# Optimization experiments

Hardware: AMD Instinct MI355X
Metric: run time of the kernel (lower is better)

Reference implementation:

```python
import jax, jax.numpy as jnp
import numpy as np

B, N = 8, 256
IN_F, OUT_F = 64, 64
IN_E, OUT_E = 32, 64  # out_edges must equal out_features (batched matmul constraint)


def setup_inputs() -> dict:
    key = jax.random.key(0)
    ks = jax.random.split(key, 9)
    s = 0.05
    return {
        "A": jax.random.uniform(ks[0], (B, N, N), dtype=jnp.float32),
        "emb_node": jax.random.normal(ks[1], (B, N, IN_F), dtype=jnp.float32),
        "emb_edge": jax.random.normal(ks[2], (B, N, N, IN_E), dtype=jnp.float32),
        "W_node": jax.random.normal(ks[3], (IN_F, OUT_F), dtype=jnp.float32) * s,
        "b_node": jnp.zeros((OUT_F,), dtype=jnp.float32),
        "W_nodes": jax.random.normal(ks[4], (IN_F, OUT_F), dtype=jnp.float32) * s,
        "b_nodes": jnp.zeros((OUT_F,), dtype=jnp.float32),
        "W_edge": jax.random.normal(ks[5], (IN_E, OUT_E), dtype=jnp.float32) * s,
        "b_edge": jnp.zeros((OUT_E,), dtype=jnp.float32),
    }


def reference(A, emb_node, emb_edge, W_node, b_node, W_nodes, b_nodes, W_edge, b_edge):
    # Dense projections (last-axis matmul, like keras Dense)
    node_x = emb_node @ W_node + b_node        # [B,N,F]
    node_sx = emb_node @ W_nodes + b_nodes     # [B,N,F]
    edge_x = emb_edge @ W_edge + b_edge        # [B,N,N,E] (E == F)
    # Fused edge-weighted aggregation: original materializes A[...,None]*edge_x
    # then does a per-channel batched matmul with node_x; same math as:
    #   node_out[b,n,f] = sum_m A[b,n,m] * edge_x[b,n,m,f] * node_x[b,m,f]
    agg = jnp.einsum('bnm,bnmf,bmf->bnf', A, edge_x, node_x)
    node_out = jax.nn.relu(agg) + jax.nn.relu(node_sx)
    edge_out = jax.nn.relu(edge_x)
    return node_out, edge_out
```

## Files before the change

kernel.cpp:

```cpp
#include <hip/hip_runtime.h>

#define BB    8
#define NN    256
#define INF   64
#define OUTF  64
#define INE   32
#define OUTE  64

using f4     = __attribute__((ext_vector_type(4))) float;
using f32x4  = __attribute__((ext_vector_type(4))) float;
using bf16x8 = __attribute__((ext_vector_type(8))) short;
using us4    = __attribute__((ext_vector_type(4))) unsigned short;

__device__ float g_node_x[BB * NN * OUTF];
__device__ float g_relu_sx[BB * NN * OUTF];

static __device__ __forceinline__ unsigned short f2bf(float x) {
    unsigned u = __builtin_bit_cast(unsigned, x);
    u += 0x7fffu + ((u >> 16) & 1u);
    return (unsigned short)(u >> 16);
}

__global__ __launch_bounds__(256) void node_proj(
    const float* __restrict__ emb_node,
    const float* __restrict__ W1, const float* __restrict__ b1,
    const float* __restrict__ W2, const float* __restrict__ b2)
{
    __shared__ float sW1[64][64];
    __shared__ float sW2[64][64];
    __shared__ float sE[4][64];

    const int tid = threadIdx.x;

    const f4* w1v = (const f4*)W1;
    const f4* w2v = (const f4*)W2;
    f4* s1 = (f4*)&sW1[0][0];
    f4* s2 = (f4*)&sW2[0][0];
#pragma unroll
    for (int i = 0; i < 4; ++i) {
        s1[tid + i * 256] = w1v[tid + i * 256];
        s2[tid + i * 256] = w2v[tid + i * 256];
    }
    const int row0 = blockIdx.x * 4;
    if (tid < 64) ((f4*)&sE[0][0])[tid] = ((const f4*)(emb_node + row0 * 64))[tid];
    __syncthreads();

    const int s = tid >> 6;
    const int f = tid & 63;
    float a1 = b1[f];
    float a2 = b2[f];
#pragma unroll
    for (int k = 0; k < 64; ++k) {
        const float e = sE[s][k];
        a1 = fmaf(e, sW1[k][f], a1);
        a2 = fmaf(e, sW2[k][f], a2);
    }
    const int row = row0 + s;
    g_node_x[row * 64 + f]  = a1;
    g_relu_sx[row * 64 + f] = fmaxf(a2, 0.f);
}

__global__ __launch_bounds__(512, 4) void edge_agg(
    const float* __restrict__ A,
    const float* __restrict__ emb_edge,
    const float* __restrict__ W_edge,
    const float* __restrict__ b_edge,
    float* __restrict__ node_out,
    float* __restrict__ edge_out)
{
    __shared__ unsigned short sEb[256][32];
    __shared__ unsigned short sWt[64][32];
    __shared__ float sA[256];
    __shared__ float sRed[8][64];

    const int tid = threadIdx.x;
    const int bn  = blockIdx.x;
    const int b   = bn >> 8;

    const f4* embv = (const f4*)(emb_edge + (size_t)bn * (NN * INE));
#pragma unroll
    for (int it = 0; it < 4; ++it) {
        const int i = tid + it * 512;
        const f4 v = __builtin_nontemporal_load(embv + i);
        us4 h;
        h.x = f2bf(v.x); h.y = f2bf(v.y); h.z = f2bf(v.z); h.w = f2bf(v.w);
        *(us4*)&sEb[i >> 3][(i & 7) * 4] = h;
    }
    {
        const int f  = tid >> 3;
        const int k0 = (tid & 7) * 4;
        us4 h;
        h.x = f2bf(W_edge[(k0 + 0) * 64 + f]);
        h.y = f2bf(W_edge[(k0 + 1) * 64 + f]);
        h.z = f2bf(W_edge[(k0 + 2) * 64 + f]);
        h.w = f2bf(W_edge[(k0 + 3) * 64 + f]);
        *(us4*)&sWt[f][k0] = h;
    }
    if (tid < 64) ((f4*)sA)[tid] = ((const f4*)(A + bn * NN))[tid];

    const int wave  = tid >> 6;
    const int lane  = tid & 63;
    const int lrow  = lane >> 4;
    const int lcol  = lane & 15;
    const int mbase = wave * 32;

    float bias[4];
#pragma unroll
    for (int ft = 0; ft < 4; ++ft) bias[ft] = b_edge[ft * 16 + lcol];

    __syncthreads();

    bf16x8 afrag[2];
#pragma unroll
    for (int mt = 0; mt < 2; ++mt)
        afrag[mt] = *(const bf16x8*)&sEb[mbase + mt * 16 + lcol][lrow * 8];
    bf16x8 bfrag[4];
#pragma unroll
    for (int ft = 0; ft < 4; ++ft)
        bfrag[ft] = *(const bf16x8*)&sWt[ft * 16 + lcol][lrow * 8];

    f32x4 acc[2][4];
#pragma unroll
    for (int mt = 0; mt < 2; ++mt)
#pragma unroll
        for (int ft = 0; ft < 4; ++ft) {
            f32x4 c; c[0] = bias[ft]; c[1] = bias[ft]; c[2] = bias[ft]; c[3] = bias[ft];
            acc[mt][ft] = __builtin_amdgcn_mfma_f32_16x16x32_bf16(
                afrag[mt], bfrag[ft], c, 0, 0, 0);
        }

    const float* nx = g_node_x + b * (NN * OUTF);
    float* eoutBase = edge_out + (size_t)bn * (NN * OUTE);
    float agg[4] = {0.f, 0.f, 0.f, 0.f};
#pragma unroll
    for (int mt = 0; mt < 2; ++mt) {
#pragma unroll
        for (int r = 0; r < 4; ++r) {
            const int m = mbase + mt * 16 + lrow * 4 + r;
            const float a = sA[m];
            const float* nxr = nx + m * 64 + lcol;
            float* er = eoutBase + (size_t)m * 64 + lcol;
#pragma unroll
            for (int ft = 0; ft < 4; ++ft) {
                const float v = acc[mt][ft][r];
                __builtin_nontemporal_store(fmaxf(v, 0.f), er + ft * 16);
                agg[ft] = fmaf(a * v, nxr[ft * 16], agg[ft]);
            }
        }
    }

#pragma unroll
    for (int ft = 0; ft < 4; ++ft) {
        float v = agg[ft];
        v += __shfl_xor(v, 16);
        v += __shfl_xor(v, 32);
        agg[ft] = v;
    }
    if (lane < 16) {
#pragma unroll
        for (int ft = 0; ft < 4; ++ft) sRed[wave][ft * 16 + lane] = agg[ft];
    }
    __syncthreads();

    if (tid < 64) {
        float s = 0.f;
#pragma unroll
        for (int w = 0; w < 8; ++w) s += sRed[w][tid];
        node_out[bn * 64 + tid] = fmaxf(s, 0.f) + g_relu_sx[bn * 64 + tid];
    }
}

extern "C" void kernel_launch(void* const* d_in, const int* in_sizes, int n_in,
                              void* d_out, int out_size, void* d_ws, size_t ws_size,
                              hipStream_t stream) {
    const float* A        = (const float*)d_in[0];
    const float* emb_node = (const float*)d_in[1];
    const float* emb_edge = (const float*)d_in[2];
    const float* W_node   = (const float*)d_in[3];
    const float* b_node   = (const float*)d_in[4];
    const float* W_nodes  = (const float*)d_in[5];
    const float* b_nodes  = (const float*)d_in[6];
    const float* W_edge   = (const float*)d_in[7];
    const float* b_edge   = (const float*)d_in[8];

    float* node_out = (float*)d_out;
    float* edge_out = node_out + BB * NN * OUTF;

    node_proj<<<(BB * NN) / 4, 256, 0, stream>>>(emb_node, W_node, b_node, W_nodes, b_nodes);
    edge_agg<<<BB * NN, 512, 0, stream>>>(A, emb_edge, W_edge, b_edge, node_out, edge_out);
}
```

Measured before the change: 59.55 us.

## Load MFMA fragments directly from global and swap operands for vectorized stores

Measured after the change: 71.65 us. 20.3% more time.

```diff
diff --git a/kernel.cpp b/kernel.cpp
--- a/kernel.cpp
+++ b/kernel.cpp
@@ -5,15 +5,14 @@
 #define INF   64
 #define OUTF  64
 #define INE   32
-#define OUTE  64
 
 using f4     = __attribute__((ext_vector_type(4))) float;
 using f32x4  = __attribute__((ext_vector_type(4))) float;
 using bf16x8 = __attribute__((ext_vector_type(8))) short;
-using us4    = __attribute__((ext_vector_type(4))) unsigned short;
 
-__device__ float g_node_x[BB * NN * OUTF];
-__device__ float g_relu_sx[BB * NN * OUTF];
+__device__ float          g_node_x[BB * NN * OUTF];
+__device__ float          g_relu_sx[BB * NN * OUTF];
+__device__ unsigned short g_wtb[OUTF * INE];
 
 static __device__ __forceinline__ unsigned short f2bf(float x) {
     unsigned u = __builtin_bit_cast(unsigned, x);
@@ -24,13 +23,22 @@
 __global__ __launch_bounds__(256) void node_proj(
     const float* __restrict__ emb_node,
     const float* __restrict__ W1, const float* __restrict__ b1,
-    const float* __restrict__ W2, const float* __restrict__ b2)
+    const float* __restrict__ W2, const float* __restrict__ b2,
+    const float* __restrict__ W_edge)
 {
     __shared__ float sW1[64][64];
     __shared__ float sW2[64][64];
     __shared__ float sE[4][64];
 
     const int tid = threadIdx.x;
+
+    if (blockIdx.x == 0) {
+        const int f  = tid >> 2;
+        const int k0 = (tid & 3) * 8;
+#pragma unroll
+        for (int j = 0; j < 8; ++j)
+            g_wtb[f * INE + k0 + j] = f2bf(W_edge[(k0 + j) * OUTF + f]);
+    }
 
     const f4* w1v = (const f4*)W1;
     const f4* w2v = (const f4*)W2;
@@ -60,105 +68,96 @@
     g_relu_sx[row * 64 + f] = fmaxf(a2, 0.f);
 }
 
-__global__ __launch_bounds__(512, 4) void edge_agg(
+__global__ __launch_bounds__(512) void edge_agg(
     const float* __restrict__ A,
     const float* __restrict__ emb_edge,
-    const float* __restrict__ W_edge,
     const float* __restrict__ b_edge,
     float* __restrict__ node_out,
     float* __restrict__ edge_out)
 {
-    __shared__ unsigned short sEb[256][32];
-    __shared__ unsigned short sWt[64][32];
-    __shared__ float sA[256];
     __shared__ float sRed[8][64];
 
-    const int tid = threadIdx.x;
-    const int bn  = blockIdx.x;
-    const int b   = bn >> 8;
-
-    const f4* embv = (const f4*)(emb_edge + (size_t)bn * (NN * INE));
-#pragma unroll
-    for (int it = 0; it < 4; ++it) {
-        const int i = tid + it * 512;
-        const f4 v = __builtin_nontemporal_load(embv + i);
-        us4 h;
-        h.x = f2bf(v.x); h.y = f2bf(v.y); h.z = f2bf(v.z); h.w = f2bf(v.w);
-        *(us4*)&sEb[i >> 3][(i & 7) * 4] = h;
-    }
-    {
-        const int f  = tid >> 3;
-        const int k0 = (tid & 7) * 4;
-        us4 h;
-        h.x = f2bf(W_edge[(k0 + 0) * 64 + f]);
-        h.y = f2bf(W_edge[(k0 + 1) * 64 + f]);
-        h.z = f2bf(W_edge[(k0 + 2) * 64 + f]);
-        h.w = f2bf(W_edge[(k0 + 3) * 64 + f]);
-        *(us4*)&sWt[f][k0] = h;
-    }
-    if (tid < 64) ((f4*)sA)[tid] = ((const f4*)(A + bn * NN))[tid];
-
-    const int wave  = tid >> 6;
-    const int lane  = tid & 63;
-    const int lrow  = lane >> 4;
-    const int lcol  = lane & 15;
+    const int tid  = threadIdx.x;
+    const int bn   = blockIdx.x;
+    const int b    = bn >> 8;
+    const int wave = tid >> 6;
+    const int lane = tid & 63;
+    const int c    = lane & 15;
+    const int q    = lane >> 4;
     const int mbase = wave * 32;
 
-    float bias[4];
+    bf16x8 efrag[2];
 #pragma unroll
-    for (int ft = 0; ft < 4; ++ft) bias[ft] = b_edge[ft * 16 + lcol];
+    for (int mt = 0; mt < 2; ++mt) {
+        const float* rp = emb_edge + (size_t)bn * (NN * INE)
+                        + (mbase + mt * 16 + c) * INE + q * 8;
+        const f4 lo = __builtin_nontemporal_load((const f4*)rp);
+        const f4 hi = __builtin_nontemporal_load((const f4*)rp + 1);
+        bf16x8 e;
+        e[0] = (short)f2bf(lo.x); e[1] = (short)f2bf(lo.y);
+        e[2] = (short)f2bf(lo.z); e[3] = (short)f2bf(lo.w);
+        e[4] = (short)f2bf(hi.x); e[5] = (short)f2bf(hi.y);
+        e[6] = (short)f2bf(hi.z); e[7] = (short)f2bf(hi.w);
+        efrag[mt] = e;
+    }
 
-    __syncthreads();
-
-    bf16x8 afrag[2];
-#pragma unroll
-    for (int mt = 0; mt < 2; ++mt)
-        afrag[mt] = *(const bf16x8*)&sEb[mbase + mt * 16 + lcol][lrow * 8];
-    bf16x8 bfrag[4];
+    bf16x8 wfrag[4];
 #pragma unroll
     for (int ft = 0; ft < 4; ++ft)
-        bfrag[ft] = *(const bf16x8*)&sWt[ft * 16 + lcol][lrow * 8];
+        wfrag[ft] = *(const bf16x8*)&g_wtb[(ft * 16 + c) * INE + q * 8];
 
     f32x4 acc[2][4];
 #pragma unroll
-    for (int mt = 0; mt < 2; ++mt)
+    for (int ft = 0; ft < 4; ++ft) {
+        const f4 bias = *(const f4*)&b_edge[ft * 16 + q * 4];
+#pragma unroll
+        for (int mt = 0; mt < 2; ++mt)
+            acc[mt][ft] = __builtin_amdgcn_mfma_f32_16x16x32_bf16(
+                wfrag[ft], efrag[mt], bias, 0, 0, 0);
+    }
+
+    const float* Arow = A + bn * NN;
+    const float* nx   = g_node_x + b * (NN * OUTF);
+    float* eo = edge_out + (size_t)bn * (NN * OUTF);
+
+    f4 agg[4];
+#pragma unroll
+    for (int ft = 0; ft < 4; ++ft) { agg[ft].x = 0.f; agg[ft].y = 0.f; agg[ft].z = 0.f; agg[ft].w = 0.f; }
+
+#pragma unroll
+    for (int mt = 0; mt < 2; ++mt) {
+        const int   m = mbase + mt * 16 + c;
+        const float a = Arow[m];
 #pragma unroll
         for (int ft = 0; ft < 4; ++ft) {
-            f32x4 c; c[0] = bias[ft]; c[1] = bias[ft]; c[2] = bias[ft]; c[3] = bias[ft];
-            acc[mt][ft] = __builtin_amdgcn_mfma_f32_16x16x32_bf16(
-                afrag[mt], bfrag[ft], c, 0, 0, 0);
-        }
-
-    const float* nx = g_node_x + b * (NN * OUTF);
-    float* eoutBase = edge_out + (size_t)bn * (NN * OUTE);
-    float agg[4] = {0.f, 0.f, 0.f, 0.f};
-#pragma unroll
-    for (int mt = 0; mt < 2; ++mt) {
-#pragma unroll
-        for (int r = 0; r < 4; ++r) {
-            const int m = mbase + mt * 16 + lrow * 4 + r;
-            const float a = sA[m];
-            const float* nxr = nx + m * 64 + lcol;
-            float* er = eoutBase + (size_t)m * 64 + lcol;
-#pragma unroll
-            for (int ft = 0; ft < 4; ++ft) {
-                const float v = acc[mt][ft][r];
-                __builtin_nontemporal_store(fmaxf(v, 0.f), er + ft * 16);
-                agg[ft] = fmaf(a * v, nxr[ft * 16], agg[ft]);
-            }
+            const int fb  = ft * 16 + q * 4;
+            const f4  v   = acc[mt][ft];
+            const f4  nxv = *(const f4*)&nx[m * OUTF + fb];
+            f4 st;
+            st.x = fmaxf(v.x, 0.f); st.y = fmaxf(v.y, 0.f);
+            st.z = fmaxf(v.z, 0.f); st.w = fmaxf(v.w, 0.f);
+            *(f4*)&eo[(size_t)m * OUTF + fb] = st;
+            agg[ft].x = fmaf(a * v.x, nxv.x, agg[ft].x);
+            agg[ft].y = fmaf(a * v.y, nxv.y, agg[ft].y);
+            agg[ft].z = fmaf(a * v.z, nxv.z, agg[ft].z);
+            agg[ft].w = fmaf(a * v.w, nxv.w, agg[ft].w);
         }
     }
 
 #pragma unroll
     for (int ft = 0; ft < 4; ++ft) {
-        float v = agg[ft];
-        v += __shfl_xor(v, 16);
-        v += __shfl_xor(v, 32);
-        agg[ft] = v;
+#pragma unroll
+        for (int s = 1; s < 16; s <<= 1) {
+            agg[ft].x += __shfl_xor(agg[ft].x, s);
+            agg[ft].y += __shfl_xor(agg[ft].y, s);
+            agg[ft].z += __shfl_xor(agg[ft].z, s);
+            agg[ft].w += __shfl_xor(agg[ft].w, s);
+        }
     }
-    if (lane < 16) {
+    if (c == 0) {
 #pragma unroll
-        for (int ft = 0; ft < 4; ++ft) sRed[wave][ft * 16 + lane] = agg[ft];
+        for (int ft = 0; ft < 4; ++ft)
+            *(f4*)&sRed[wave][ft * 16 + q * 4] = agg[ft];
     }
     __syncthreads();
 
@@ -166,7 +165,7 @@
         float s = 0.f;
 #pragma unroll
         for (int w = 0; w < 8; ++w) s += sRed[w][tid];
-        node_out[bn * 64 + tid] = fmaxf(s, 0.f) + g_relu_sx[bn * 64 + tid];
+        node_out[bn * OUTF + tid] = fmaxf(s, 0.f) + g_relu_sx[bn * OUTF + tid];
     }
 }
 
@@ -186,6 +185,7 @@
     float* node_out = (float*)d_out;
     float* edge_out = node_out + BB * NN * OUTF;
 
-    node_proj<<<(BB * NN) / 4, 256, 0, stream>>>(emb_node, W_node, b_node, W_nodes, b_nodes);
-    edge_agg<<<BB * NN, 512, 0, stream>>>(A, emb_edge, W_edge, b_edge, node_out, edge_out);
+    node_proj<<<(BB * NN) / 4, 256, 0, stream>>>(emb_node, W_node, b_node,
+                                                 W_nodes, b_nodes, W_edge);
+    edge_agg<<<BB * NN, 512, 0, stream>>>(A, emb_edge, b_edge, node_out, edge_out);
 }
```
